# Kernel optimization log

Measured on AMD Instinct MI355X. Metric: run time of the kernel, lower is better.

Reference implementation:

```python
import jax, jax.numpy as jnp
import numpy as np


def setup_inputs() -> dict:
    key = jax.random.key(0)
    k1, k2 = jax.random.split(key)
    N, M, Q, D = 4096, 128, 64, 128
    a_embeddings = jax.random.normal(k1, (N, D), dtype=jnp.float32)
    b_embedding_sets = jax.random.normal(k2, (M, Q, D), dtype=jnp.float32)
    gaussian_variance = jnp.full((1,), 0.5, dtype=jnp.float32)  # nn.Parameter default
    return {
        "a_embeddings": a_embeddings,
        "b_embedding_sets": b_embedding_sets,
        "gaussian_variance": gaussian_variance,
    }


def reference(a_embeddings, b_embedding_sets, gaussian_variance):
    # Covariance = var * I, so inv(cov) = I / var and the Mahalanobis term is
    # ||a - mu||^2 / var. Expand the squared distance to avoid the NxMxQxD
    # broadcast intermediate the torch code materializes (same math).
    inv_var = 1.0 / gaussian_variance[0]
    a2 = jnp.sum(a_embeddings * a_embeddings, axis=-1)          # [N]
    b2 = jnp.sum(b_embedding_sets * b_embedding_sets, axis=-1)  # [M, Q]
    ab = jnp.einsum("nd,mqd->nmq", a_embeddings, b_embedding_sets)  # [N, M, Q]
    x2 = (a2[:, None, None] - 2.0 * ab + b2[None, :, :]) * inv_var  # [N, M, Q]
    densities = jnp.exp(-0.5 * x2)                  # [N, M, Q]
    dens_per_cluster = densities.sum(axis=2)        # [N, M]
    prob = dens_per_cluster / (dens_per_cluster.sum(axis=1, keepdims=True) + 1e-10)
    return prob
```

## Files before the change

kernel.cpp:

```cpp
#include <hip/hip_runtime.h>
#include <hip/hip_bf16.h>
#include <math.h>

#define NN 4096
#define MM 128
#define QQ 64
#define DD 128
#define CC (MM * QQ)

typedef float f32x4 __attribute__((ext_vector_type(4)));
typedef int   i32x4 __attribute__((ext_vector_type(4)));
typedef int   i32x8 __attribute__((ext_vector_type(8)));

#define AS1 __attribute__((address_space(1)))
#define AS3 __attribute__((address_space(3)))

__global__ __launch_bounds__(256)
void prep_kernel(const float* __restrict__ A, const float* __restrict__ B,
                 unsigned char* __restrict__ A8, unsigned char* __restrict__ B8,
                 float* __restrict__ a2, float* __restrict__ b2)
{
    const int row = blockIdx.x * 8 + (threadIdx.x >> 5);
    const int l32 = threadIdx.x & 31;
    const float* src;
    unsigned char* dst;
    float* nrm;
    if (row < NN) { src = A + (size_t)row * DD; dst = A8 + (size_t)row * DD; nrm = a2 + row; }
    else {
        int r = row - NN;
        src = B + (size_t)r * DD; dst = B8 + (size_t)r * DD; nrm = b2 + r;
    }
    float4 v = ((const float4*)src)[l32];
    int pk = __builtin_amdgcn_cvt_pk_fp8_f32(v.x, v.y, 0, false);
    pk     = __builtin_amdgcn_cvt_pk_fp8_f32(v.z, v.w, pk, true);
    ((int*)dst)[l32] = pk;
    float s = v.x * v.x + v.y * v.y + v.z * v.z + v.w * v.w;
    #pragma unroll
    for (int m = 16; m > 0; m >>= 1) s += __shfl_xor(s, m, 64);
    if (l32 == 0) *nrm = s;
}

__global__ __launch_bounds__(256, 3)
void kde_dens_kernel(const unsigned char* __restrict__ A8,
                     const unsigned char* __restrict__ B8,
                     const float* __restrict__ var,
                     const float* __restrict__ a2w,
                     const float* __restrict__ b2w,
                     float* __restrict__ dpc)
{
    __shared__ unsigned char As[128 * DD];
    __shared__ unsigned char Bs[128 * DD];
    __shared__ float a2s[128];
    __shared__ float b2s[128];
    __shared__ float red[4][64];

    const int lin = blockIdx.x;
    const int xcd = lin & 7;
    const int loc = lin >> 3;
    const int cb  = (xcd << 3) | (loc & 7);
    const int nb  = loc >> 3;
    const int n0  = nb * 128;
    const int c0  = cb * 128;

    const int t = threadIdx.x, w = t >> 6, lane = t & 63;

    {
        const unsigned char* Ab = A8 + (size_t)n0 * DD;
        const unsigned char* Bb = B8 + (size_t)c0 * DD;
        #pragma unroll
        for (int i = 0; i < 4; ++i) {
            const int slot = w * 256 + i * 64 + lane;
            const int r = slot >> 3, c16 = slot & 7, scb = c16 ^ (r & 7);
            __builtin_amdgcn_global_load_lds(
                (const AS1 unsigned int*)(Ab + r * DD + scb * 16),
                (AS3 unsigned int*)&As[slot * 16], 16, 0, 0);
            __builtin_amdgcn_global_load_lds(
                (const AS1 unsigned int*)(Bb + r * DD + scb * 16),
                (AS3 unsigned int*)&Bs[slot * 16], 16, 0, 0);
        }
        if (t < 128)        a2s[t]       = a2w[n0 + t];
        else                b2s[t - 128] = b2w[c0 + (t - 128)];
    }
    __syncthreads();

    const int l15 = lane & 15, q = lane >> 4, xr = l15 & 7;
    const int wy = w >> 1, wx = w & 1;
    const int rbase = wy * 64, cbase = wx * 64;

    i32x8 a8[4];
    #pragma unroll
    for (int i = 0; i < 4; ++i) {
        const int ro = (rbase + i * 16 + l15) * DD;
        const i32x4 lo = *(const i32x4*)&As[ro + (((q << 1) | 0) ^ xr) * 16];
        const i32x4 hi = *(const i32x4*)&As[ro + (((q << 1) | 1) ^ xr) * 16];
        #pragma unroll
        for (int e = 0; e < 4; ++e) { a8[i][e] = lo[e]; a8[i][4 + e] = hi[e]; }
    }

    f32x4 acc[4][4] = {};
    #pragma unroll
    for (int j = 0; j < 4; ++j) {
        const int ro = (cbase + j * 16 + l15) * DD;
        const i32x4 lo = *(const i32x4*)&Bs[ro + (((q << 1) | 0) ^ xr) * 16];
        const i32x4 hi = *(const i32x4*)&Bs[ro + (((q << 1) | 1) ^ xr) * 16];
        i32x8 b8;
        #pragma unroll
        for (int e = 0; e < 4; ++e) { b8[e] = lo[e]; b8[4 + e] = hi[e]; }
        #pragma unroll
        for (int i = 0; i < 4; ++i)
            acc[i][j] = __builtin_amdgcn_mfma_scale_f32_16x16x128_f8f6f4(
                            a8[i], b8, acc[i][j],
                            0, 0,
                            0, 127,
                            0, 127);
    }

    const float hinv = 0.5f / var[0];
    float rowsum[4][4];
    #pragma unroll
    for (int i = 0; i < 4; ++i) {
        #pragma unroll
        for (int reg = 0; reg < 4; ++reg) {
            const float a2 = a2s[rbase + i * 16 + q * 4 + reg];
            float p = 0.f;
            #pragma unroll
            for (int j = 0; j < 4; ++j) {
                const float b2 = b2s[cbase + j * 16 + l15];
                p += __expf((2.f * acc[i][j][reg] - a2 - b2) * hinv);
            }
            rowsum[i][reg] = p;
        }
    }
    #pragma unroll
    for (int mask = 1; mask < 16; mask <<= 1)
        #pragma unroll
        for (int i = 0; i < 4; ++i)
            #pragma unroll
            for (int reg = 0; reg < 4; ++reg)
                rowsum[i][reg] += __shfl_xor(rowsum[i][reg], mask, 64);

    if (l15 == 0) {
        #pragma unroll
        for (int i = 0; i < 4; ++i) {
            f32x4 o = {rowsum[i][0], rowsum[i][1], rowsum[i][2], rowsum[i][3]};
            *(f32x4*)&red[w][i * 16 + q * 4] = o;
        }
    }
    const int m = (cb << 1) + wx;
    dpc[(size_t)m * NN + n0 + rbase + lane] = red[w][lane];
}

__global__ __launch_bounds__(1024)
void kde_norm_kernel(const float* __restrict__ dpc, float* __restrict__ out)
{
    __shared__ float tile[MM][65];
    __shared__ float rden[64];
    const int n0 = blockIdx.x * 64;
    const int t  = threadIdx.x;

    #pragma unroll
    for (int it = 0; it < 2; ++it) {
        const int m  = (t >> 4) + it * 64;
        const int nc = (t & 15) * 4;
        float4 v = *(const float4*)&dpc[(size_t)m * NN + n0 + nc];
        tile[m][nc]     = v.x;
        tile[m][nc + 1] = v.y;
        tile[m][nc + 2] = v.z;
        tile[m][nc + 3] = v.w;
    }
    __syncthreads();

    if (t < 64) {
        float s = 0.f;
        #pragma unroll 8
        for (int m = 0; m < MM; ++m) s += tile[m][t];
        rden[t] = 1.f / (s + 1e-10f);
    }
    __syncthreads();

    const int nloc = t >> 4;
    const int m0   = (t & 15) * 8;
    const float r  = rden[nloc];
    float4 o0, o1;
    o0.x = tile[m0][nloc] * r;     o0.y = tile[m0 + 1][nloc] * r;
    o0.z = tile[m0 + 2][nloc] * r; o0.w = tile[m0 + 3][nloc] * r;
    o1.x = tile[m0 + 4][nloc] * r; o1.y = tile[m0 + 5][nloc] * r;
    o1.z = tile[m0 + 6][nloc] * r; o1.w = tile[m0 + 7][nloc] * r;
    float* obase = &out[(size_t)(n0 + nloc) * MM + m0];
    *(float4*)obase       = o0;
    *(float4*)(obase + 4) = o1;
}

extern "C" void kernel_launch(void* const* d_in, const int* in_sizes, int n_in,
                              void* d_out, int out_size, void* d_ws, size_t ws_size,
                              hipStream_t stream) {
    const float* A   = (const float*)d_in[0];
    const float* B   = (const float*)d_in[1];
    const float* var = (const float*)d_in[2];
    float* out = (float*)d_out;

    unsigned char* A8 = (unsigned char*)d_ws;
    unsigned char* B8 = A8 + (size_t)NN * DD;
    float* a2  = (float*)(B8 + (size_t)CC * DD);
    float* b2  = a2 + NN;
    float* dpc = b2 + CC;

    prep_kernel<<<(NN + CC) / 8, 256, 0, stream>>>(A, B, A8, B8, a2, b2);
    kde_dens_kernel<<<2048, 256, 0, stream>>>(A8, B8, var, a2, b2, dpc);
    kde_norm_kernel<<<NN / 64, 1024, 0, stream>>>(dpc, out);
}
```

Baseline: 79.28 us.

## Fuse prep, density and normalize stages into one persistent kernel with grid barriers

Replaces three kernel launches with a single persistent kernel of 512 blocks that runs fp8 conversion, the MFMA density pass and the normalization in sequence, separated by software grid barriers built on atomics. Each block keeps its B tile resident in LDS and loops over four A tiles, double-buffering the next A tile with async global-to-LDS loads. The aim is to remove launch gaps, reuse B across A tiles, and overlap loads with compute. In exchange it adds barrier spin latency and an extra memset per call, and correctness depends on all 512 blocks being co-resident.

```diff
diff --git a/kernel.cpp b/kernel.cpp
--- a/kernel.cpp
+++ b/kernel.cpp
@@ -1,5 +1,4 @@
 #include <hip/hip_runtime.h>
-#include <hip/hip_bf16.h>
 #include <math.h>
 
 #define NN 4096
@@ -7,6 +6,7 @@
 #define QQ 64
 #define DD 128
 #define CC (MM * QQ)
+#define GRIDN 512
 
 typedef float f32x4 __attribute__((ext_vector_type(4)));
 typedef int   i32x4 __attribute__((ext_vector_type(4)));
@@ -15,180 +15,220 @@
 #define AS1 __attribute__((address_space(1)))
 #define AS3 __attribute__((address_space(3)))
 
-__global__ __launch_bounds__(256)
-void prep_kernel(const float* __restrict__ A, const float* __restrict__ B,
-                 unsigned char* __restrict__ A8, unsigned char* __restrict__ B8,
-                 float* __restrict__ a2, float* __restrict__ b2)
+__device__ __forceinline__ void grid_barrier(unsigned* cnt)
 {
-    const int row = blockIdx.x * 8 + (threadIdx.x >> 5);
-    const int l32 = threadIdx.x & 31;
-    const float* src;
-    unsigned char* dst;
-    float* nrm;
-    if (row < NN) { src = A + (size_t)row * DD; dst = A8 + (size_t)row * DD; nrm = a2 + row; }
-    else {
-        int r = row - NN;
-        src = B + (size_t)r * DD; dst = B8 + (size_t)r * DD; nrm = b2 + r;
-    }
-    float4 v = ((const float4*)src)[l32];
-    int pk = __builtin_amdgcn_cvt_pk_fp8_f32(v.x, v.y, 0, false);
-    pk     = __builtin_amdgcn_cvt_pk_fp8_f32(v.z, v.w, pk, true);
-    ((int*)dst)[l32] = pk;
-    float s = v.x * v.x + v.y * v.y + v.z * v.z + v.w * v.w;
-    #pragma unroll
-    for (int m = 16; m > 0; m >>= 1) s += __shfl_xor(s, m, 64);
-    if (l32 == 0) *nrm = s;
+    __syncthreads();
+    if (threadIdx.x == 0) {
+        __threadfence();
+        const unsigned arrived =
+            __hip_atomic_fetch_add(cnt, 1u, __ATOMIC_ACQ_REL, __HIP_MEMORY_SCOPE_AGENT);
+        if (arrived + 1u < (unsigned)GRIDN) {
+            while (__hip_atomic_load(cnt, __ATOMIC_ACQUIRE, __HIP_MEMORY_SCOPE_AGENT)
+                   < (unsigned)GRIDN)
+                __builtin_amdgcn_s_sleep(2);
+        }
+        __threadfence();
+    }
+    __syncthreads();
 }
 
-__global__ __launch_bounds__(256, 3)
-void kde_dens_kernel(const unsigned char* __restrict__ A8,
-                     const unsigned char* __restrict__ B8,
-                     const float* __restrict__ var,
-                     const float* __restrict__ a2w,
-                     const float* __restrict__ b2w,
-                     float* __restrict__ dpc)
+__global__ __launch_bounds__(256, 2)
+void kde_fused(const float* __restrict__ A, const float* __restrict__ B,
+               const float* __restrict__ var,
+               unsigned char* __restrict__ A8, unsigned char* __restrict__ B8,
+               float* __restrict__ a2w, float* __restrict__ b2w,
+               float* __restrict__ dpc,
+               float* __restrict__ out,
+               unsigned* __restrict__ bar)
 {
-    __shared__ unsigned char As[128 * DD];
     __shared__ unsigned char Bs[128 * DD];
-    __shared__ float a2s[128];
+    __shared__ unsigned char As[2][128 * DD];
+    __shared__ float a2s[2][128];
     __shared__ float b2s[128];
     __shared__ float red[4][64];
 
-    const int lin = blockIdx.x;
-    const int xcd = lin & 7;
-    const int loc = lin >> 3;
-    const int cb  = (xcd << 3) | (loc & 7);
-    const int nb  = loc >> 3;
-    const int n0  = nb * 128;
-    const int c0  = cb * 128;
-
+    const int bid = blockIdx.x;
     const int t = threadIdx.x, w = t >> 6, lane = t & 63;
 
     {
-        const unsigned char* Ab = A8 + (size_t)n0 * DD;
-        const unsigned char* Bb = B8 + (size_t)c0 * DD;
+        const int l32 = t & 31;
         #pragma unroll
-        for (int i = 0; i < 4; ++i) {
-            const int slot = w * 256 + i * 64 + lane;
-            const int r = slot >> 3, c16 = slot & 7, scb = c16 ^ (r & 7);
-            __builtin_amdgcn_global_load_lds(
-                (const AS1 unsigned int*)(Ab + r * DD + scb * 16),
-                (AS3 unsigned int*)&As[slot * 16], 16, 0, 0);
-            __builtin_amdgcn_global_load_lds(
-                (const AS1 unsigned int*)(Bb + r * DD + scb * 16),
-                (AS3 unsigned int*)&Bs[slot * 16], 16, 0, 0);
-        }
-        if (t < 128)        a2s[t]       = a2w[n0 + t];
-        else                b2s[t - 128] = b2w[c0 + (t - 128)];
-    }
-    __syncthreads();
-
-    const int l15 = lane & 15, q = lane >> 4, xr = l15 & 7;
-    const int wy = w >> 1, wx = w & 1;
-    const int rbase = wy * 64, cbase = wx * 64;
-
-    i32x8 a8[4];
-    #pragma unroll
-    for (int i = 0; i < 4; ++i) {
-        const int ro = (rbase + i * 16 + l15) * DD;
-        const i32x4 lo = *(const i32x4*)&As[ro + (((q << 1) | 0) ^ xr) * 16];
-        const i32x4 hi = *(const i32x4*)&As[ro + (((q << 1) | 1) ^ xr) * 16];
+        for (int p = 0; p < 3; ++p) {
+            const int row = bid * 24 + p * 8 + (t >> 5);
+            const float* src; unsigned char* dst; float* nrm;
+            if (row < NN) { src = A + (size_t)row * DD; dst = A8 + (size_t)row * DD; nrm = a2w + row; }
+            else {
+                const int r = row - NN;
+                src = B + (size_t)r * DD; dst = B8 + (size_t)r * DD; nrm = b2w + r;
+            }
+            const float4 v = ((const float4*)src)[l32];
+            int pk = __builtin_amdgcn_cvt_pk_fp8_f32(v.x, v.y, 0, false);
+            pk     = __builtin_amdgcn_cvt_pk_fp8_f32(v.z, v.w, pk, true);
+            ((int*)dst)[l32] = pk;
+            float s = v.x * v.x + v.y * v.y + v.z * v.z + v.w * v.w;
+            #pragma unroll
+            for (int mth = 16; mth > 0; mth >>= 1) s += __shfl_xor(s, mth, 64);
+            if (l32 == 0) *nrm = s;
+        }
+    }
+
+    grid_barrier(&bar[0]);
+
+    {
+        const int xcd = bid & 7;
+        const int cb  = (xcd << 3) | ((bid >> 3) & 7);
+        const int nb0 = bid >> 6;
+        const int c0  = cb * 128;
+
+        {
+            const unsigned char* Bb = B8 + (size_t)c0 * DD;
+            #pragma unroll
+            for (int i = 0; i < 4; ++i) {
+                const int slot = w * 256 + i * 64 + lane;
+                const int r = slot >> 3, c16 = slot & 7, scb = c16 ^ (r & 7);
+                __builtin_amdgcn_global_load_lds(
+                    (const AS1 unsigned int*)(Bb + r * DD + scb * 16),
+                    (AS3 unsigned int*)&Bs[slot * 16], 16, 0, 0);
+            }
+            if (w >= 2)
+                __builtin_amdgcn_global_load_lds(
+                    (const AS1 unsigned int*)(b2w + c0 + (w - 2) * 64 + lane),
+                    (AS3 unsigned int*)&b2s[(w - 2) * 64 + lane], 4, 0, 0);
+            const int n0 = nb0 * 128;
+            const unsigned char* Ab = A8 + (size_t)n0 * DD;
+            #pragma unroll
+            for (int i = 0; i < 4; ++i) {
+                const int slot = w * 256 + i * 64 + lane;
+                const int r = slot >> 3, c16 = slot & 7, scb = c16 ^ (r & 7);
+                __builtin_amdgcn_global_load_lds(
+                    (const AS1 unsigned int*)(Ab + r * DD + scb * 16),
+                    (AS3 unsigned int*)&As[0][slot * 16], 16, 0, 0);
+            }
+            if (w < 2)
+                __builtin_amdgcn_global_load_lds(
+                    (const AS1 unsigned int*)(a2w + n0 + w * 64 + lane),
+                    (AS3 unsigned int*)&a2s[0][w * 64 + lane], 4, 0, 0);
+        }
+        __syncthreads();
+
+        const int l15 = lane & 15, q = lane >> 4, xr = l15 & 7;
+        const int wy = w >> 1, wx = w & 1;
+        const int rbase = wy * 64, cbase = wx * 64;
+        const int m = (cb << 1) + wx;
+        const float hinv = 0.5f / var[0];
+
         #pragma unroll
-        for (int e = 0; e < 4; ++e) { a8[i][e] = lo[e]; a8[i][4 + e] = hi[e]; }
-    }
-
-    f32x4 acc[4][4] = {};
-    #pragma unroll
-    for (int j = 0; j < 4; ++j) {
-        const int ro = (cbase + j * 16 + l15) * DD;
-        const i32x4 lo = *(const i32x4*)&Bs[ro + (((q << 1) | 0) ^ xr) * 16];
-        const i32x4 hi = *(const i32x4*)&Bs[ro + (((q << 1) | 1) ^ xr) * 16];
-        i32x8 b8;
-        #pragma unroll
-        for (int e = 0; e < 4; ++e) { b8[e] = lo[e]; b8[4 + e] = hi[e]; }
-        #pragma unroll
-        for (int i = 0; i < 4; ++i)
-            acc[i][j] = __builtin_amdgcn_mfma_scale_f32_16x16x128_f8f6f4(
-                            a8[i], b8, acc[i][j],
-                            0, 0,
-                            0, 127,
-                            0, 127);
-    }
-
-    const float hinv = 0.5f / var[0];
-    float rowsum[4][4];
-    #pragma unroll
-    for (int i = 0; i < 4; ++i) {
-        #pragma unroll
-        for (int reg = 0; reg < 4; ++reg) {
-            const float a2 = a2s[rbase + i * 16 + q * 4 + reg];
-            float p = 0.f;
+        for (int t4 = 0; t4 < 4; ++t4) {
+            const int buf = t4 & 1;
+            const int n0  = (nb0 + 8 * t4) * 128;
+
+            if (t4 < 3) {
+                const int n0n = (nb0 + 8 * (t4 + 1)) * 128;
+                const unsigned char* Ab = A8 + (size_t)n0n * DD;
+                #pragma unroll
+                for (int i = 0; i < 4; ++i) {
+                    const int slot = w * 256 + i * 64 + lane;
+                    const int r = slot >> 3, c16 = slot & 7, scb = c16 ^ (r & 7);
+                    __builtin_amdgcn_global_load_lds(
+                        (const AS1 unsigned int*)(Ab + r * DD + scb * 16),
+                        (AS3 unsigned int*)&As[buf ^ 1][slot * 16], 16, 0, 0);
+                }
+                if (w < 2)
+                    __builtin_amdgcn_global_load_lds(
+                        (const AS1 unsigned int*)(a2w + n0n + w * 64 + lane),
+                        (AS3 unsigned int*)&a2s[buf ^ 1][w * 64 + lane], 4, 0, 0);
+            }
+
+            i32x8 a8[4];
+            #pragma unroll
+            for (int i = 0; i < 4; ++i) {
+                const int ro = (rbase + i * 16 + l15) * DD;
+                const i32x4 lo = *(const i32x4*)&As[buf][ro + (((q << 1) | 0) ^ xr) * 16];
+                const i32x4 hi = *(const i32x4*)&As[buf][ro + (((q << 1) | 1) ^ xr) * 16];
+                #pragma unroll
+                for (int e = 0; e < 4; ++e) { a8[i][e] = lo[e]; a8[i][4 + e] = hi[e]; }
+            }
+
+            f32x4 acc[4][4] = {};
             #pragma unroll
             for (int j = 0; j < 4; ++j) {
-                const float b2 = b2s[cbase + j * 16 + l15];
-                p += __expf((2.f * acc[i][j][reg] - a2 - b2) * hinv);
-            }
-            rowsum[i][reg] = p;
-        }
-    }
-    #pragma unroll
-    for (int mask = 1; mask < 16; mask <<= 1)
-        #pragma unroll
-        for (int i = 0; i < 4; ++i)
-            #pragma unroll
-            for (int reg = 0; reg < 4; ++reg)
-                rowsum[i][reg] += __shfl_xor(rowsum[i][reg], mask, 64);
-
-    if (l15 == 0) {
-        #pragma unroll
-        for (int i = 0; i < 4; ++i) {
-            f32x4 o = {rowsum[i][0], rowsum[i][1], rowsum[i][2], rowsum[i][3]};
-            *(f32x4*)&red[w][i * 16 + q * 4] = o;
-        }
-    }
-    const int m = (cb << 1) + wx;
-    dpc[(size_t)m * NN + n0 + rbase + lane] = red[w][lane];
-}
-
-__global__ __launch_bounds__(1024)
-void kde_norm_kernel(const float* __restrict__ dpc, float* __restrict__ out)
-{
-    __shared__ float tile[MM][65];
-    __shared__ float rden[64];
-    const int n0 = blockIdx.x * 64;
-    const int t  = threadIdx.x;
-
-    #pragma unroll
-    for (int it = 0; it < 2; ++it) {
-        const int m  = (t >> 4) + it * 64;
-        const int nc = (t & 15) * 4;
-        float4 v = *(const float4*)&dpc[(size_t)m * NN + n0 + nc];
-        tile[m][nc]     = v.x;
-        tile[m][nc + 1] = v.y;
-        tile[m][nc + 2] = v.z;
-        tile[m][nc + 3] = v.w;
-    }
-    __syncthreads();
-
-    if (t < 64) {
-        float s = 0.f;
-        #pragma unroll 8
-        for (int m = 0; m < MM; ++m) s += tile[m][t];
-        rden[t] = 1.f / (s + 1e-10f);
-    }
-    __syncthreads();
-
-    const int nloc = t >> 4;
-    const int m0   = (t & 15) * 8;
-    const float r  = rden[nloc];
-    float4 o0, o1;
-    o0.x = tile[m0][nloc] * r;     o0.y = tile[m0 + 1][nloc] * r;
-    o0.z = tile[m0 + 2][nloc] * r; o0.w = tile[m0 + 3][nloc] * r;
-    o1.x = tile[m0 + 4][nloc] * r; o1.y = tile[m0 + 5][nloc] * r;
-    o1.z = tile[m0 + 6][nloc] * r; o1.w = tile[m0 + 7][nloc] * r;
-    float* obase = &out[(size_t)(n0 + nloc) * MM + m0];
-    *(float4*)obase       = o0;
-    *(float4*)(obase + 4) = o1;
+                const int ro = (cbase + j * 16 + l15) * DD;
+                const i32x4 lo = *(const i32x4*)&Bs[ro + (((q << 1) | 0) ^ xr) * 16];
+                const i32x4 hi = *(const i32x4*)&Bs[ro + (((q << 1) | 1) ^ xr) * 16];
+                i32x8 b8;
+                #pragma unroll
+                for (int e = 0; e < 4; ++e) { b8[e] = lo[e]; b8[4 + e] = hi[e]; }
+                #pragma unroll
+                for (int i = 0; i < 4; ++i)
+                    acc[i][j] = __builtin_amdgcn_mfma_scale_f32_16x16x128_f8f6f4(
+                                    a8[i], b8, acc[i][j],
+                                    0, 0,
+                                    0, 127,
+                                    0, 127);
+            }
+
+            float rowsum[4][4];
+            #pragma unroll
+            for (int i = 0; i < 4; ++i) {
+                #pragma unroll
+                for (int reg = 0; reg < 4; ++reg) {
+                    const float a2v = a2s[buf][rbase + i * 16 + q * 4 + reg];
+                    float p = 0.f;
+                    #pragma unroll
+                    for (int j = 0; j < 4; ++j) {
+                        const float b2v = b2s[cbase + j * 16 + l15];
+                        p += __expf((2.f * acc[i][j][reg] - a2v - b2v) * hinv);
+                    }
+                    rowsum[i][reg] = p;
+                }
+            }
+            #pragma unroll
+            for (int mask = 1; mask < 16; mask <<= 1)
+                #pragma unroll
+                for (int i = 0; i < 4; ++i)
+                    #pragma unroll
+                    for (int reg = 0; reg < 4; ++reg)
+                        rowsum[i][reg] += __shfl_xor(rowsum[i][reg], mask, 64);
+
+            if (l15 == 0) {
+                #pragma unroll
+                for (int i = 0; i < 4; ++i) {
+                    f32x4 o = {rowsum[i][0], rowsum[i][1], rowsum[i][2], rowsum[i][3]};
+                    *(f32x4*)&red[w][i * 16 + q * 4] = o;
+                }
+            }
+            dpc[(size_t)m * NN + n0 + rbase + lane] = red[w][lane];
+            __syncthreads();
+        }
+    }
+
+    grid_barrier(&bar[1]);
+
+    {
+        const int n0c = bid * 8;
+        float* tile = (float*)&As[0][0];
+        float* rden = &red[0][0];
+        const int mr = t >> 1, half = t & 1;
+        const float4 v = *(const float4*)&dpc[(size_t)mr * NN + n0c + half * 4];
+        float* tr = &tile[mr * 9 + half * 4];
+        tr[0] = v.x; tr[1] = v.y; tr[2] = v.z; tr[3] = v.w;
+        __syncthreads();
+        if (t < 8) {
+            float s = 0.f;
+            #pragma unroll 8
+            for (int mm = 0; mm < MM; ++mm) s += tile[mm * 9 + t];
+            rden[t] = 1.f / (s + 1e-10f);
+        }
+        __syncthreads();
+        const int j = t >> 5, mq = (t & 31) * 4;
+        const float r = rden[j];
+        float4 o;
+        o.x = tile[(mq + 0) * 9 + j] * r;
+        o.y = tile[(mq + 1) * 9 + j] * r;
+        o.z = tile[(mq + 2) * 9 + j] * r;
+        o.w = tile[(mq + 3) * 9 + j] * r;
+        *(float4*)&out[(size_t)(n0c + j) * MM + mq] = o;
+    }
 }
 
 extern "C" void kernel_launch(void* const* d_in, const int* in_sizes, int n_in,
@@ -204,8 +244,8 @@
     float* a2  = (float*)(B8 + (size_t)CC * DD);
     float* b2  = a2 + NN;
     float* dpc = b2 + CC;
-
-    prep_kernel<<<(NN + CC) / 8, 256, 0, stream>>>(A, B, A8, B8, a2, b2);
-    kde_dens_kernel<<<2048, 256, 0, stream>>>(A8, B8, var, a2, b2, dpc);
-    kde_norm_kernel<<<NN / 64, 1024, 0, stream>>>(dpc, out);
+    unsigned* bar = (unsigned*)((char*)d_ws + (4u << 20));
+
+    hipMemsetAsync(bar, 0, 64, stream);
+    kde_fused<<<GRIDN, 256, 0, stream>>>(A, B, var, A8, B8, a2, b2, dpc, out, bar);
 }
```

Result: slower. 168.4 us (+112.5%).

## Swap MFMA operands to reduce cluster sums in-register and shrink norm blocks

Applied to the files above, without the earlier changes.

The dens kernel swaps the MFMA A/B operands so each lane's accumulator registers run along the cluster dimension. The per-row sum over Q then happens mostly inside registers plus two cross-lane shuffles, replacing four shuffle stages and an LDS staging buffer. The exponent math is folded into exp2 with precomputed scaled norms, and the kernel uses setprio around the MFMA block. The norm kernel moves to 256-thread blocks covering 16 rows each, giving more blocks and smaller LDS tiles, at the cost of shorter contiguous loads.

```diff
diff --git a/kernel.cpp b/kernel.cpp
--- a/kernel.cpp
+++ b/kernel.cpp
@@ -1,5 +1,4 @@
 #include <hip/hip_runtime.h>
-#include <hip/hip_bf16.h>
 #include <math.h>
 
 #define NN 4096
@@ -52,7 +51,6 @@
     __shared__ unsigned char Bs[128 * DD];
     __shared__ float a2s[128];
     __shared__ float b2s[128];
-    __shared__ float red[4][64];
 
     const int lin = blockIdx.x;
     const int xcd = lin & 7;
@@ -86,6 +84,22 @@
     const int l15 = lane & 15, q = lane >> 4, xr = l15 & 7;
     const int wy = w >> 1, wx = w & 1;
     const int rbase = wy * 64, cbase = wx * 64;
+    const int m = (cb << 1) + wx;
+    const float hinvL = (0.5f / var[0]) * 1.44269504088896f;
+    const float h2L   = hinvL + hinvL;
+
+    f32x4 nbh[4];
+    i32x8 b8v[4];
+    #pragma unroll
+    for (int jc = 0; jc < 4; ++jc) {
+        const f32x4 bv = *(const f32x4*)&b2s[cbase + jc * 16 + q * 4];
+        nbh[jc] = -bv * hinvL;
+        const int ro = (cbase + jc * 16 + l15) * DD;
+        const i32x4 lo = *(const i32x4*)&Bs[ro + (((q << 1) | 0) ^ xr) * 16];
+        const i32x4 hi = *(const i32x4*)&Bs[ro + (((q << 1) | 1) ^ xr) * 16];
+        #pragma unroll
+        for (int e = 0; e < 4; ++e) { b8v[jc][e] = lo[e]; b8v[jc][4 + e] = hi[e]; }
+    }
 
     i32x8 a8[4];
     #pragma unroll
@@ -98,95 +112,76 @@
     }
 
     f32x4 acc[4][4] = {};
-    #pragma unroll
-    for (int j = 0; j < 4; ++j) {
-        const int ro = (cbase + j * 16 + l15) * DD;
-        const i32x4 lo = *(const i32x4*)&Bs[ro + (((q << 1) | 0) ^ xr) * 16];
-        const i32x4 hi = *(const i32x4*)&Bs[ro + (((q << 1) | 1) ^ xr) * 16];
-        i32x8 b8;
-        #pragma unroll
-        for (int e = 0; e < 4; ++e) { b8[e] = lo[e]; b8[4 + e] = hi[e]; }
+    __builtin_amdgcn_s_setprio(1);
+    #pragma unroll
+    for (int jc = 0; jc < 4; ++jc)
         #pragma unroll
         for (int i = 0; i < 4; ++i)
-            acc[i][j] = __builtin_amdgcn_mfma_scale_f32_16x16x128_f8f6f4(
-                            a8[i], b8, acc[i][j],
+            acc[jc][i] = __builtin_amdgcn_mfma_scale_f32_16x16x128_f8f6f4(
+                            b8v[jc], a8[i], acc[jc][i],
                             0, 0,
                             0, 127,
                             0, 127);
-    }
-
-    const float hinv = 0.5f / var[0];
-    float rowsum[4][4];
+    __builtin_amdgcn_s_setprio(0);
+
+    float sums[4];
     #pragma unroll
     for (int i = 0; i < 4; ++i) {
-        #pragma unroll
-        for (int reg = 0; reg < 4; ++reg) {
-            const float a2 = a2s[rbase + i * 16 + q * 4 + reg];
-            float p = 0.f;
+        const float aih = a2s[rbase + i * 16 + l15] * hinvL;
+        float s0 = 0.f, s1 = 0.f;
+        #pragma unroll
+        for (int jc = 0; jc < 4; jc += 2) {
             #pragma unroll
-            for (int j = 0; j < 4; ++j) {
-                const float b2 = b2s[cbase + j * 16 + l15];
-                p += __expf((2.f * acc[i][j][reg] - a2 - b2) * hinv);
+            for (int r = 0; r < 4; ++r) {
+                s0 += __builtin_amdgcn_exp2f(fmaf(h2L, acc[jc][i][r],     nbh[jc][r]     - aih));
+                s1 += __builtin_amdgcn_exp2f(fmaf(h2L, acc[jc + 1][i][r], nbh[jc + 1][r] - aih));
             }
-            rowsum[i][reg] = p;
         }
-    }
-    #pragma unroll
-    for (int mask = 1; mask < 16; mask <<= 1)
-        #pragma unroll
-        for (int i = 0; i < 4; ++i)
-            #pragma unroll
-            for (int reg = 0; reg < 4; ++reg)
-                rowsum[i][reg] += __shfl_xor(rowsum[i][reg], mask, 64);
-
-    if (l15 == 0) {
-        #pragma unroll
-        for (int i = 0; i < 4; ++i) {
-            f32x4 o = {rowsum[i][0], rowsum[i][1], rowsum[i][2], rowsum[i][3]};
-            *(f32x4*)&red[w][i * 16 + q * 4] = o;
-        }
-    }
-    const int m = (cb << 1) + wx;
-    dpc[(size_t)m * NN + n0 + rbase + lane] = red[w][lane];
-}
-
-__global__ __launch_bounds__(1024)
+        float s = s0 + s1;
+        s += __shfl_xor(s, 16, 64);
+        s += __shfl_xor(s, 32, 64);
+        sums[i] = s;
+    }
+    const float v01 = (q & 1) ? sums[1] : sums[0];
+    const float v23 = (q & 1) ? sums[3] : sums[2];
+    const float myv = (q & 2) ? v23 : v01;
+    dpc[(size_t)m * NN + n0 + rbase + lane] = myv;
+}
+
+__global__ __launch_bounds__(256)
 void kde_norm_kernel(const float* __restrict__ dpc, float* __restrict__ out)
 {
-    __shared__ float tile[MM][65];
-    __shared__ float rden[64];
-    const int n0 = blockIdx.x * 64;
+    __shared__ float tile[128][17];
+    __shared__ float rden[16];
+    const int n0 = blockIdx.x * 16;
     const int t  = threadIdx.x;
 
-    #pragma unroll
-    for (int it = 0; it < 2; ++it) {
-        const int m  = (t >> 4) + it * 64;
-        const int nc = (t & 15) * 4;
-        float4 v = *(const float4*)&dpc[(size_t)m * NN + n0 + nc];
-        tile[m][nc]     = v.x;
-        tile[m][nc + 1] = v.y;
-        tile[m][nc + 2] = v.z;
-        tile[m][nc + 3] = v.w;
+    const int mr = t >> 1, half = t & 1;
+    {
+        const float4 va = *(const float4*)&dpc[(size_t)mr * NN + n0 + half * 8];
+        const float4 vb = *(const float4*)&dpc[(size_t)mr * NN + n0 + half * 8 + 4];
+        float* tr = &tile[mr][half * 8];
+        tr[0] = va.x; tr[1] = va.y; tr[2] = va.z; tr[3] = va.w;
+        tr[4] = vb.x; tr[5] = vb.y; tr[6] = vb.z; tr[7] = vb.w;
     }
     __syncthreads();
 
-    if (t < 64) {
+    if (t < 16) {
         float s = 0.f;
         #pragma unroll 8
-        for (int m = 0; m < MM; ++m) s += tile[m][t];
+        for (int mm = 0; mm < MM; ++mm) s += tile[mm][t];
         rden[t] = 1.f / (s + 1e-10f);
     }
     __syncthreads();
 
-    const int nloc = t >> 4;
-    const int m0   = (t & 15) * 8;
-    const float r  = rden[nloc];
+    const int j = t >> 4, m0 = (t & 15) * 8;
+    const float r = rden[j];
     float4 o0, o1;
-    o0.x = tile[m0][nloc] * r;     o0.y = tile[m0 + 1][nloc] * r;
-    o0.z = tile[m0 + 2][nloc] * r; o0.w = tile[m0 + 3][nloc] * r;
-    o1.x = tile[m0 + 4][nloc] * r; o1.y = tile[m0 + 5][nloc] * r;
-    o1.z = tile[m0 + 6][nloc] * r; o1.w = tile[m0 + 7][nloc] * r;
-    float* obase = &out[(size_t)(n0 + nloc) * MM + m0];
+    o0.x = tile[m0][j] * r;     o0.y = tile[m0 + 1][j] * r;
+    o0.z = tile[m0 + 2][j] * r; o0.w = tile[m0 + 3][j] * r;
+    o1.x = tile[m0 + 4][j] * r; o1.y = tile[m0 + 5][j] * r;
+    o1.z = tile[m0 + 6][j] * r; o1.w = tile[m0 + 7][j] * r;
+    float* obase = &out[(size_t)(n0 + j) * MM + m0];
     *(float4*)obase       = o0;
     *(float4*)(obase + 4) = o1;
 }
@@ -207,5 +202,5 @@
 
     prep_kernel<<<(NN + CC) / 8, 256, 0, stream>>>(A, B, A8, B8, a2, b2);
     kde_dens_kernel<<<2048, 256, 0, stream>>>(A8, B8, var, a2, b2, dpc);
-    kde_norm_kernel<<<NN / 64, 1024, 0, stream>>>(dpc, out);
-}
+    kde_norm_kernel<<<NN / 16, 256, 0, stream>>>(dpc, out);
+}
```

After: 76.80 us (median of 2 runs). -3.1%, faster.
